# Kernel tuning notes

Hardware: AMD Instinct MI355X
Metric: run time of the kernel (lower is better)

Reference implementation:

```python
import jax, jax.numpy as jnp
import numpy as np

N_NODES = 100000


def gcn_conv(x, src, dst, deg_inv_sqrt, W, b, n):
    # GCNConv: h = D^{-1/2} (A + I) D^{-1/2} (x W) + b
    h = x @ W                                   # [N, out]
    norm = deg_inv_sqrt[src] * deg_inv_sqrt[dst]  # [E+N]
    msg = h[src] * norm[:, None]                # gather + scale
    out = jax.ops.segment_sum(msg, dst, num_segments=n)  # scatter-add
    return out + b


def setup_inputs() -> dict:
    key = jax.random.key(0)
    k1, k2, k3, k4 = jax.random.split(key, 4)
    N, E, IN, H, C = N_NODES, 1600000, 256, 128, 16
    x = jax.random.normal(k1, (N, IN), dtype=jnp.float32)
    edge_index = jax.random.randint(k2, (2, E), 0, N, dtype=jnp.int64)
    W1 = jax.random.normal(k3, (IN, H), dtype=jnp.float32) * (1.0 / np.sqrt(IN))
    b1 = jnp.zeros((H,), dtype=jnp.float32)
    W2 = jax.random.normal(k4, (H, C), dtype=jnp.float32) * (1.0 / np.sqrt(H))
    b2 = jnp.zeros((C,), dtype=jnp.float32)
    return {"x": x, "edge_index": edge_index, "W1": W1, "b1": b1, "W2": W2, "b2": b2}


def reference(x, edge_index, W1, b1, W2, b2):
    n = x.shape[0]
    loop = jnp.arange(n, dtype=edge_index.dtype)
    src = jnp.concatenate([edge_index[0], loop])  # add self-loops
    dst = jnp.concatenate([edge_index[1], loop])
    deg = jax.ops.segment_sum(jnp.ones_like(src, dtype=x.dtype), dst, num_segments=n)
    deg_inv_sqrt = jax.lax.rsqrt(deg)  # deg >= 1 due to self-loops

    h = gcn_conv(x, src, dst, deg_inv_sqrt, W1, b1, n)
    h = jax.nn.relu(h)
    # dropout is identity in eval mode
    out = gcn_conv(h, src, dst, deg_inv_sqrt, W2, b2, n)
    return jax.nn.log_softmax(out, axis=1)
```

## Files before the change

kernel.cpp:

```cpp
#include <hip/hip_runtime.h>
#include <math.h>

#define IN_DIM 256
#define H_DIM  128
#define C_DIM  16
#define BK_SHIFT 8
#define BK_CAP   6144
#define CHUNK    4096

typedef __attribute__((ext_vector_type(8))) short bf16x8;
typedef __attribute__((ext_vector_type(4))) float f32x4;

__device__ __forceinline__ ushort f2bf(float f) {
    uint u = __float_as_uint(f);
    u += 0x7fffu + ((u >> 16) & 1u);
    return (ushort)(u >> 16);
}
__device__ __forceinline__ float bflo(uint v) { return __uint_as_float(v << 16); }
__device__ __forceinline__ float bfhi(uint v) { return __uint_as_float(v & 0xffff0000u); }
__device__ __forceinline__ uint pk2(float a, float b) {
    return (uint)f2bf(a) | ((uint)f2bf(b) << 16);
}

__global__ void k_zero(int* __restrict__ p, int n) {
    int i = blockIdx.x * blockDim.x + threadIdx.x;
    if (i < n) p[i] = 0;
}

__global__ __launch_bounds__(256) void k_part(const int* __restrict__ esrc, const int* __restrict__ edst, int E,
                                              int* __restrict__ bcnt, int2* __restrict__ part) {
    __shared__ int sh_cnt[512];
    __shared__ int sh_base[512];
    __shared__ int sh_gbase[512];
    __shared__ int sh_scan[256];
    __shared__ int2 sh_rec[CHUNK];
    int t = threadIdx.x;
    int c0 = blockIdx.x * CHUNK;
    int cnt = min(CHUNK, E - c0);
    sh_cnt[t] = 0; sh_cnt[t + 256] = 0;
    __syncthreads();
    int srcv[16], dstv[16], lrank[16];
#pragma unroll
    for (int j = 0; j < 16; j++) {
        int li = j * 256 + t;
        if (li < cnt) {
            srcv[j] = esrc[c0 + li]; dstv[j] = edst[c0 + li];
            lrank[j] = atomicAdd(&sh_cnt[dstv[j] >> BK_SHIFT], 1);
        }
    }
    __syncthreads();
    int pairsum = sh_cnt[2 * t] + sh_cnt[2 * t + 1];
    sh_scan[t] = pairsum;
    __syncthreads();
    for (int off = 1; off < 256; off <<= 1) {
        int x = 0;
        if (t >= off) x = sh_scan[t - off];
        __syncthreads();
        if (t >= off) sh_scan[t] += x;
        __syncthreads();
    }
    int excl = sh_scan[t] - pairsum;
    sh_base[2 * t] = excl;
    sh_base[2 * t + 1] = excl + sh_cnt[2 * t];
    __syncthreads();
    for (int b = t; b < 512; b += 256) {
        int c = sh_cnt[b];
        if (c > 0) sh_gbase[b] = atomicAdd(&bcnt[b], c);
    }
#pragma unroll
    for (int j = 0; j < 16; j++) {
        int li = j * 256 + t;
        if (li < cnt) {
            int b = dstv[j] >> BK_SHIFT;
            sh_rec[sh_base[b] + lrank[j]] = make_int2(srcv[j], dstv[j]);
        }
    }
    __syncthreads();
    for (int idx = t; idx < cnt; idx += 256) {
        int2 r = sh_rec[idx];
        int b = r.y >> BK_SHIFT;
        int pos = sh_gbase[b] + (idx - sh_base[b]);
        if (pos < BK_CAP) part[(size_t)b * BK_CAP + pos] = r;
    }
}

__global__ __launch_bounds__(256) void k_bdeg(const int* __restrict__ bcnt, const int2* __restrict__ part,
                                              int* __restrict__ deg, float* __restrict__ dis, int N) {
    __shared__ int hist[256];
    int b = blockIdx.x, t = threadIdx.x;
    hist[t] = 0;
    __syncthreads();
    int cnt = bcnt[b];
    const int2* bp = &part[(size_t)b * BK_CAP];
    for (int idx = t; idx < cnt; idx += 256)
        atomicAdd(&hist[bp[idx].y & 255], 1);
    __syncthreads();
    int node = b * 256 + t;
    if (node < N) {
        deg[node] = hist[t];
        dis[node] = rsqrtf((float)(hist[t] + 1));
    }
}

__global__ void k_scanA(const int* __restrict__ deg, int* __restrict__ bsums, int N) {
    __shared__ int sh[256];
    int b = blockIdx.x, t = threadIdx.x;
    int i0 = b * 2048 + t * 8;
    int s = 0;
#pragma unroll
    for (int j = 0; j < 8; j++) { int i = i0 + j; s += (i < N) ? deg[i] : 0; }
    sh[t] = s; __syncthreads();
    for (int off = 128; off > 0; off >>= 1) {
        if (t < off) sh[t] += sh[t + off];
        __syncthreads();
    }
    if (t == 0) bsums[b] = sh[0];
}

__global__ void k_scanB(int* __restrict__ bsums, int nb, int* __restrict__ offsets, int N) {
    if (threadIdx.x == 0 && blockIdx.x == 0) {
        int run = 0;
        for (int b = 0; b < nb; b++) { int v = bsums[b]; bsums[b] = run; run += v; }
        offsets[N] = run;
    }
}

__global__ void k_scanC(const int* __restrict__ deg, const int* __restrict__ bsums,
                        int* __restrict__ offsets, int N) {
    __shared__ int sh[256];
    int b = blockIdx.x, t = threadIdx.x;
    int base = bsums[b];
    int i0 = b * 2048 + t * 8;
    int v[8], loc[8]; int s = 0;
#pragma unroll
    for (int j = 0; j < 8; j++) { int i = i0 + j; v[j] = (i < N) ? deg[i] : 0; loc[j] = s; s += v[j]; }
    sh[t] = s; __syncthreads();
    for (int off = 1; off < 256; off <<= 1) {
        int x = 0;
        if (t >= off) x = sh[t - off];
        __syncthreads();
        if (t >= off) sh[t] += x;
        __syncthreads();
    }
    int tb = base + ((t > 0) ? sh[t - 1] : 0);
#pragma unroll
    for (int j = 0; j < 8; j++) {
        int i = i0 + j;
        if (i < N) offsets[i] = tb + loc[j];
    }
}

__global__ __launch_bounds__(256) void k_bsort(const int* __restrict__ bcnt, const int2* __restrict__ part,
                                               const float* __restrict__ dis, const int* __restrict__ offsets,
                                               int2* __restrict__ csr) {
    __shared__ int hist[256];
    __shared__ int run[256];
    __shared__ int2 srt[BK_CAP];
    int b = blockIdx.x, t = threadIdx.x;
    hist[t] = 0;
    __syncthreads();
    int cnt = min(bcnt[b], BK_CAP);
    const int2* bp = &part[(size_t)b * BK_CAP];
    for (int idx = t; idx < cnt; idx += 256)
        atomicAdd(&hist[bp[idx].y & 255], 1);
    __syncthreads();
    int v = hist[t];
    run[t] = v;
    __syncthreads();
    for (int off = 1; off < 256; off <<= 1) {
        int x = 0;
        if (t >= off) x = run[t - off];
        __syncthreads();
        if (t >= off) run[t] += x;
        __syncthreads();
    }
    int start = run[t] - v;
    __syncthreads();
    run[t] = start;
    __syncthreads();
    for (int idx = t; idx < cnt; idx += 256) {
        int2 r = bp[idx];
        int n = r.y & 255;
        int lpos = atomicAdd(&run[n], 1);
        float w = dis[r.x];
        srt[lpos] = make_int2(r.x, __float_as_int(w));
    }
    __syncthreads();
    int segbase = offsets[b * 256];
    for (int idx = t; idx < cnt; idx += 256)
        csr[segbase + idx] = srt[idx];
}

__global__ void k_w1cast(const float* __restrict__ W1, ushort* __restrict__ W1T) {
    int n = blockIdx.x, k = threadIdx.x;
    W1T[n * 256 + k] = f2bf(W1[k * 128 + n]);
}

__global__ __launch_bounds__(256) void k_gemm1(const float* __restrict__ x,
                                               const ushort* __restrict__ W1T,
                                               ushort* __restrict__ h1, int N) {
    __shared__ ushort Al[128 * 64];
    __shared__ ushort Bl[128 * 64];
    int tid = threadIdx.x;
    int lane = tid & 63, wid = tid >> 6;
    int wr = wid >> 1, wc = wid & 1;
    int r0 = blockIdx.x * 128;
    int row16 = lane & 15, kgrp = lane >> 4;

    f32x4 acc[4][4];
#pragma unroll
    for (int i = 0; i < 4; i++)
#pragma unroll
        for (int j = 0; j < 4; j++) acc[i][j] = (f32x4){0.f, 0.f, 0.f, 0.f};

    int srow = tid >> 1, shalf = tid & 1;

    for (int k0 = 0; k0 < 256; k0 += 64) {
        {
            int gr = r0 + srow;
            float4 f[8];
            if (gr < N) {
                const float* xp = &x[(size_t)gr * 256 + k0 + shalf * 32];
#pragma unroll
                for (int j = 0; j < 8; j++) f[j] = *(const float4*)&xp[j * 4];
            } else {
#pragma unroll
                for (int j = 0; j < 8; j++) f[j] = make_float4(0.f, 0.f, 0.f, 0.f);
            }
#pragma unroll
            for (int j = 0; j < 4; j++) {
                uint4 w;
                w.x = pk2(f[2 * j].x, f[2 * j].y);
                w.y = pk2(f[2 * j].z, f[2 * j].w);
                w.z = pk2(f[2 * j + 1].x, f[2 * j + 1].y);
                w.w = pk2(f[2 * j + 1].z, f[2 * j + 1].w);
                int idx = (srow * 64 + shalf * 32 + j * 8) ^ ((srow & 7) << 3);
                *(uint4*)&Al[idx] = w;
            }
        }
        {
            const ushort* wp = &W1T[srow * 256 + k0 + shalf * 32];
#pragma unroll
            for (int j = 0; j < 4; j++) {
                uint4 w = *(const uint4*)&wp[j * 8];
                int idx = (srow * 64 + shalf * 32 + j * 8) ^ ((srow & 7) << 3);
                *(uint4*)&Bl[idx] = w;
            }
        }
        __syncthreads();
#pragma unroll
        for (int kk = 0; kk < 2; kk++) {
            bf16x8 a[4], b[4];
#pragma unroll
            for (int mi = 0; mi < 4; mi++) {
                int r = wr * 64 + mi * 16 + row16;
                a[mi] = *(const bf16x8*)&Al[(r * 64 + kk * 32 + kgrp * 8) ^ ((r & 7) << 3)];
            }
#pragma unroll
            for (int ni = 0; ni < 4; ni++) {
                int c = wc * 64 + ni * 16 + row16;
                b[ni] = *(const bf16x8*)&Bl[(c * 64 + kk * 32 + kgrp * 8) ^ ((c & 7) << 3)];
            }
#pragma unroll
            for (int mi = 0; mi < 4; mi++)
#pragma unroll
                for (int ni = 0; ni < 4; ni++)
                    acc[mi][ni] = __builtin_amdgcn_mfma_f32_16x16x32_bf16(
                        a[mi], b[ni], acc[mi][ni], 0, 0, 0);
        }
        __syncthreads();
    }
#pragma unroll
    for (int mi = 0; mi < 4; mi++) {
        int rbase = r0 + wr * 64 + mi * 16 + kgrp * 4;
#pragma unroll
        for (int ni = 0; ni < 4; ni++) {
            int col = wc * 64 + ni * 16 + row16;
#pragma unroll
            for (int r = 0; r < 4; r++) {
                int gr = rbase + r;
                if (gr < N) h1[(size_t)gr * 128 + col] = f2bf(acc[mi][ni][r]);
            }
        }
    }
}

__global__ __launch_bounds__(256) void k_agg1(const ushort* __restrict__ h1,
                                              const float* __restrict__ dis,
                                              const int* __restrict__ off,
                                              const int2* __restrict__ csr,
                                              const float* __restrict__ b1,
                                              const float* __restrict__ W2,
                                              ushort* __restrict__ h2, int N) {
    __shared__ float sh[4][128];
    int wave = threadIdx.x >> 6;
    int lane = threadIdx.x & 63;
    int node = blockIdx.x * 4 + wave;
    if (node >= N) return;

    int grp = lane >> 4, c = lane & 15;
    float w2r[32];
#pragma unroll
    for (int j = 0; j < 32; j++) w2r[j] = W2[(grp * 32 + j) * 16 + c];
    float2 bl = *(const float2*)&b1[lane * 2];

    float dd = dis[node];
    const uint* hp = (const uint*)h1;
    uint a = hp[(size_t)node * 64 + lane];
    float accx = bflo(a) * dd, accy = bfhi(a) * dd;

    int p0 = off[node], p1 = off[node + 1];
    for (int pb = p0; pb < p1; pb += 64) {
        int rem64 = p1 - pb;
        int cnt = rem64 < 64 ? rem64 : 64;
        int s = 0; float w = 0.f;
        if (lane < cnt) { int2 e = csr[pb + lane]; s = e.x; w = __int_as_float(e.y); }
        int j = 0;
        for (; j + 8 <= cnt; j += 8) {
            uint v[8]; float ww[8];
#pragma unroll
            for (int u = 0; u < 8; u++) {
                int ss = __shfl(s, j + u);
                ww[u] = __shfl(w, j + u);
                v[u] = hp[(size_t)ss * 64 + lane];
            }
#pragma unroll
            for (int u = 0; u < 8; u++) {
                accx += bflo(v[u]) * ww[u];
                accy += bfhi(v[u]) * ww[u];
            }
        }
        int rem = cnt - j;
        if (rem) {
            uint v[8]; float ww[8];
#pragma unroll
            for (int u = 0; u < 8; u++) {
                int ss = __shfl(s, j + u);
                float t = __shfl(w, j + u);
                ww[u] = (u < rem) ? t : 0.f;
                v[u] = (u < rem) ? hp[(size_t)ss * 64 + lane] : 0u;
            }
#pragma unroll
            for (int u = 0; u < 8; u++) {
                accx += bflo(v[u]) * ww[u];
                accy += bfhi(v[u]) * ww[u];
            }
        }
    }
    accx = fmaxf(accx * dd + bl.x, 0.f);
    accy = fmaxf(accy * dd + bl.y, 0.f);
    sh[wave][lane * 2]     = accx;
    sh[wave][lane * 2 + 1] = accy;
    float cs = 0.f;
#pragma unroll
    for (int j = 0; j < 32; j++) cs += sh[wave][grp * 32 + j] * w2r[j];
    cs += __shfl_xor(cs, 16);
    cs += __shfl_xor(cs, 32);
    if (lane < 16) h2[(size_t)node * 16 + lane] = f2bf(cs);
}

__global__ __launch_bounds__(256) void k_final(const ushort* __restrict__ h2,
                                               const float* __restrict__ b2,
                                               const float* __restrict__ dis,
                                               const int* __restrict__ off,
                                               const int2* __restrict__ csr,
                                               float* __restrict__ out, int N) {
    int g = threadIdx.x >> 2;
    int q = threadIdx.x & 3;
    int node = blockIdx.x * 64 + g;
    if (node >= N) return;
    float dd = dis[node];
    uint2 v0 = *(const uint2*)&h2[(size_t)node * 16 + q * 4];
    float a0 = bflo(v0.x) * dd, a1 = bfhi(v0.x) * dd;
    float a2 = bflo(v0.y) * dd, a3 = bfhi(v0.y) * dd;
    int p0 = off[node], p1 = off[node + 1];
    for (int pb = p0; pb < p1; pb += 4) {
        int rem4 = p1 - pb;
        int cnt = rem4 < 4 ? rem4 : 4;
        int s = 0; float w = 0.f;
        if (q < cnt) { int2 e = csr[pb + q]; s = e.x; w = __int_as_float(e.y); }
        uint2 vv[4]; float ww[4];
#pragma unroll
        for (int u = 0; u < 4; u++) {
            int ss = __shfl(s, u, 4);
            float t = __shfl(w, u, 4);
            ww[u] = (u < cnt) ? t : 0.f;
            if (u < cnt) vv[u] = *(const uint2*)&h2[(size_t)ss * 16 + q * 4];
            else         vv[u] = make_uint2(0u, 0u);
        }
#pragma unroll
        for (int u = 0; u < 4; u++) {
            a0 += bflo(vv[u].x) * ww[u]; a1 += bfhi(vv[u].x) * ww[u];
            a2 += bflo(vv[u].y) * ww[u]; a3 += bfhi(vv[u].y) * ww[u];
        }
    }
    a0 = a0 * dd + b2[q * 4 + 0];
    a1 = a1 * dd + b2[q * 4 + 1];
    a2 = a2 * dd + b2[q * 4 + 2];
    a3 = a3 * dd + b2[q * 4 + 3];
    float m = fmaxf(fmaxf(a0, a1), fmaxf(a2, a3));
    m = fmaxf(m, __shfl_xor(m, 1, 4));
    m = fmaxf(m, __shfl_xor(m, 2, 4));
    float s4 = expf(a0 - m) + expf(a1 - m) + expf(a2 - m) + expf(a3 - m);
    s4 += __shfl_xor(s4, 1, 4);
    s4 += __shfl_xor(s4, 2, 4);
    float l = m + logf(s4);
    f32x4 o = {a0 - l, a1 - l, a2 - l, a3 - l};
    *(f32x4*)&out[(size_t)node * 16 + q * 4] = o;
}

extern "C" void kernel_launch(void* const* d_in, const int* in_sizes, int n_in,
                              void* d_out, int out_size, void* d_ws, size_t ws_size,
                              hipStream_t stream) {
    const float* x    = (const float*)d_in[0];
    const int*   eidx = (const int*)d_in[1];
    const float* W1   = (const float*)d_in[2];
    const float* b1   = (const float*)d_in[3];
    const float* W2   = (const float*)d_in[4];
    const float* b2   = (const float*)d_in[5];
    float* out = (float*)d_out;

    int N = in_sizes[0] / IN_DIM;
    int E = in_sizes[1] / 2;
    const int* esrc = eidx;
    const int* edst = eidx + E;

    char* ws = (char*)d_ws;
    size_t wo = 0;
    auto alloc = [&](size_t bytes) -> void* {
        void* p = ws + wo;
        wo = (wo + bytes + 255) & ~(size_t)255;
        return p;
    };
    int NB = (N + 255) >> 8;

    int*    deg     = (int*)alloc((size_t)N * 4);
    float*  dis     = (float*)alloc((size_t)N * 4);
    int*    offsets = (int*)alloc((size_t)(N + 1) * 4);
    int*    bsums   = (int*)alloc(256 * 4);
    int*    bcnt    = (int*)alloc(512 * 4);
    int2*   part    = (int2*)alloc((size_t)NB * BK_CAP * 8);
    int2*   csr     = (int2*)alloc((size_t)E * 8);
    ushort* W1T     = (ushort*)alloc((size_t)IN_DIM * H_DIM * 2);
    ushort* h1      = (ushort*)alloc((size_t)N * H_DIM * 2);
    ushort* h2      = (ushort*)alloc((size_t)N * C_DIM * 2);

    int nb_scan = (N + 2047) / 2048;

    k_zero  <<<2, 256, 0, stream>>>(bcnt, 512);
    k_part  <<<(E + CHUNK - 1) / CHUNK, 256, 0, stream>>>(esrc, edst, E, bcnt, part);
    k_bdeg  <<<NB, 256, 0, stream>>>(bcnt, part, deg, dis, N);
    k_scanA <<<nb_scan, 256, 0, stream>>>(deg, bsums, N);
    k_scanB <<<1, 64, 0, stream>>>(bsums, nb_scan, offsets, N);
    k_scanC <<<nb_scan, 256, 0, stream>>>(deg, bsums, offsets, N);
    k_bsort <<<NB, 256, 0, stream>>>(bcnt, part, dis, offsets, csr);
    k_w1cast<<<H_DIM, IN_DIM, 0, stream>>>(W1, W1T);

    k_gemm1 <<<(N + 127) / 128, 256, 0, stream>>>(x, W1T, h1, N);
    k_agg1  <<<(N + 3) / 4, 256, 0, stream>>>(h1, dis, offsets, csr, b1, W2, h2, N);
    k_final <<<(N + 63) / 64, 256, 0, stream>>>(h2, b2, dis, offsets, csr, out, N);
}
```

Baseline: 191.0 us.

## Collapse degree and scan kernels into bucket scan, store CSR as src-only

Replaces the per-node degree kernel and the three-kernel prefix scan with a single-block scan over bucket counts. The bucket sort kernel now computes each node's degree, inverse sqrt degree and CSR offset from its local histogram. CSR entries shrink from (src, weight) pairs to src indices only, and the aggregation kernels gather dis[src] on the fly. This removes several launches and a full pass over the partitioned edges, and halves CSR traffic, at the cost of an extra random gather of dis per edge in both aggregation passes.

```diff
diff --git a/kernel.cpp b/kernel.cpp
--- a/kernel.cpp
+++ b/kernel.cpp
@@ -84,78 +84,34 @@
     }
 }
 
-__global__ __launch_bounds__(256) void k_bdeg(const int* __restrict__ bcnt, const int2* __restrict__ part,
-                                              int* __restrict__ deg, float* __restrict__ dis, int N) {
-    __shared__ int hist[256];
-    int b = blockIdx.x, t = threadIdx.x;
-    hist[t] = 0;
-    __syncthreads();
-    int cnt = bcnt[b];
-    const int2* bp = &part[(size_t)b * BK_CAP];
-    for (int idx = t; idx < cnt; idx += 256)
-        atomicAdd(&hist[bp[idx].y & 255], 1);
-    __syncthreads();
-    int node = b * 256 + t;
-    if (node < N) {
-        deg[node] = hist[t];
-        dis[node] = rsqrtf((float)(hist[t] + 1));
-    }
-}
-
-__global__ void k_scanA(const int* __restrict__ deg, int* __restrict__ bsums, int N) {
-    __shared__ int sh[256];
-    int b = blockIdx.x, t = threadIdx.x;
-    int i0 = b * 2048 + t * 8;
-    int s = 0;
-#pragma unroll
-    for (int j = 0; j < 8; j++) { int i = i0 + j; s += (i < N) ? deg[i] : 0; }
-    sh[t] = s; __syncthreads();
-    for (int off = 128; off > 0; off >>= 1) {
-        if (t < off) sh[t] += sh[t + off];
-        __syncthreads();
-    }
-    if (t == 0) bsums[b] = sh[0];
-}
-
-__global__ void k_scanB(int* __restrict__ bsums, int nb, int* __restrict__ offsets, int N) {
-    if (threadIdx.x == 0 && blockIdx.x == 0) {
-        int run = 0;
-        for (int b = 0; b < nb; b++) { int v = bsums[b]; bsums[b] = run; run += v; }
-        offsets[N] = run;
-    }
-}
-
-__global__ void k_scanC(const int* __restrict__ deg, const int* __restrict__ bsums,
-                        int* __restrict__ offsets, int N) {
-    __shared__ int sh[256];
-    int b = blockIdx.x, t = threadIdx.x;
-    int base = bsums[b];
-    int i0 = b * 2048 + t * 8;
-    int v[8], loc[8]; int s = 0;
-#pragma unroll
-    for (int j = 0; j < 8; j++) { int i = i0 + j; v[j] = (i < N) ? deg[i] : 0; loc[j] = s; s += v[j]; }
-    sh[t] = s; __syncthreads();
+__global__ __launch_bounds__(256) void k_bscan(const int* __restrict__ bcnt, int* __restrict__ bkbase,
+                                               int* __restrict__ offsets, int N) {
+    __shared__ int sh_scan[256];
+    int t = threadIdx.x;
+    int a0 = bcnt[2 * t], a1 = bcnt[2 * t + 1];
+    int pairsum = a0 + a1;
+    sh_scan[t] = pairsum;
+    __syncthreads();
     for (int off = 1; off < 256; off <<= 1) {
         int x = 0;
-        if (t >= off) x = sh[t - off];
-        __syncthreads();
-        if (t >= off) sh[t] += x;
-        __syncthreads();
-    }
-    int tb = base + ((t > 0) ? sh[t - 1] : 0);
-#pragma unroll
-    for (int j = 0; j < 8; j++) {
-        int i = i0 + j;
-        if (i < N) offsets[i] = tb + loc[j];
-    }
-}
-
-__global__ __launch_bounds__(256) void k_bsort(const int* __restrict__ bcnt, const int2* __restrict__ part,
-                                               const float* __restrict__ dis, const int* __restrict__ offsets,
-                                               int2* __restrict__ csr) {
+        if (t >= off) x = sh_scan[t - off];
+        __syncthreads();
+        if (t >= off) sh_scan[t] += x;
+        __syncthreads();
+    }
+    int excl = sh_scan[t] - pairsum;
+    bkbase[2 * t] = excl;
+    bkbase[2 * t + 1] = excl + a0;
+    if (t == 255) offsets[N] = sh_scan[255];
+}
+
+__global__ __launch_bounds__(256) void k_bsort(const int* __restrict__ bcnt, const int* __restrict__ bkbase,
+                                               const int2* __restrict__ part,
+                                               float* __restrict__ dis, int* __restrict__ offsets,
+                                               int* __restrict__ csr, int N) {
     __shared__ int hist[256];
     __shared__ int run[256];
-    __shared__ int2 srt[BK_CAP];
+    __shared__ int srt[BK_CAP];
     int b = blockIdx.x, t = threadIdx.x;
     hist[t] = 0;
     __syncthreads();
@@ -175,20 +131,23 @@
         __syncthreads();
     }
     int start = run[t] - v;
+    int base = bkbase[b];
+    int node = b * 256 + t;
+    if (node < N) {
+        dis[node] = rsqrtf((float)(v + 1));
+        offsets[node] = base + start;
+    }
     __syncthreads();
     run[t] = start;
     __syncthreads();
     for (int idx = t; idx < cnt; idx += 256) {
         int2 r = bp[idx];
-        int n = r.y & 255;
-        int lpos = atomicAdd(&run[n], 1);
-        float w = dis[r.x];
-        srt[lpos] = make_int2(r.x, __float_as_int(w));
-    }
-    __syncthreads();
-    int segbase = offsets[b * 256];
+        int lpos = atomicAdd(&run[r.y & 255], 1);
+        srt[lpos] = r.x;
+    }
+    __syncthreads();
     for (int idx = t; idx < cnt; idx += 256)
-        csr[segbase + idx] = srt[idx];
+        csr[base + idx] = srt[idx];
 }
 
 __global__ void k_w1cast(const float* __restrict__ W1, ushort* __restrict__ W1T) {
@@ -288,7 +247,7 @@
 __global__ __launch_bounds__(256) void k_agg1(const ushort* __restrict__ h1,
                                               const float* __restrict__ dis,
                                               const int* __restrict__ off,
-                                              const int2* __restrict__ csr,
+                                              const int* __restrict__ csr,
                                               const float* __restrict__ b1,
                                               const float* __restrict__ W2,
                                               ushort* __restrict__ h2, int N) {
@@ -314,7 +273,7 @@
         int rem64 = p1 - pb;
         int cnt = rem64 < 64 ? rem64 : 64;
         int s = 0; float w = 0.f;
-        if (lane < cnt) { int2 e = csr[pb + lane]; s = e.x; w = __int_as_float(e.y); }
+        if (lane < cnt) { s = csr[pb + lane]; w = dis[s]; }
         int j = 0;
         for (; j + 8 <= cnt; j += 8) {
             uint v[8]; float ww[8];
@@ -363,7 +322,7 @@
                                                const float* __restrict__ b2,
                                                const float* __restrict__ dis,
                                                const int* __restrict__ off,
-                                               const int2* __restrict__ csr,
+                                               const int* __restrict__ csr,
                                                float* __restrict__ out, int N) {
     int g = threadIdx.x >> 2;
     int q = threadIdx.x & 3;
@@ -378,7 +337,7 @@
         int rem4 = p1 - pb;
         int cnt = rem4 < 4 ? rem4 : 4;
         int s = 0; float w = 0.f;
-        if (q < cnt) { int2 e = csr[pb + q]; s = e.x; w = __int_as_float(e.y); }
+        if (q < cnt) { s = csr[pb + q]; w = dis[s]; }
         uint2 vv[4]; float ww[4];
 #pragma unroll
         for (int u = 0; u < 4; u++) {
@@ -434,26 +393,20 @@
     };
     int NB = (N + 255) >> 8;
 
-    int*    deg     = (int*)alloc((size_t)N * 4);
     float*  dis     = (float*)alloc((size_t)N * 4);
     int*    offsets = (int*)alloc((size_t)(N + 1) * 4);
-    int*    bsums   = (int*)alloc(256 * 4);
     int*    bcnt    = (int*)alloc(512 * 4);
+    int*    bkbase  = (int*)alloc(512 * 4);
     int2*   part    = (int2*)alloc((size_t)NB * BK_CAP * 8);
-    int2*   csr     = (int2*)alloc((size_t)E * 8);
+    int*    csr     = (int*)alloc((size_t)E * 4);
     ushort* W1T     = (ushort*)alloc((size_t)IN_DIM * H_DIM * 2);
     ushort* h1      = (ushort*)alloc((size_t)N * H_DIM * 2);
     ushort* h2      = (ushort*)alloc((size_t)N * C_DIM * 2);
 
-    int nb_scan = (N + 2047) / 2048;
-
     k_zero  <<<2, 256, 0, stream>>>(bcnt, 512);
     k_part  <<<(E + CHUNK - 1) / CHUNK, 256, 0, stream>>>(esrc, edst, E, bcnt, part);
-    k_bdeg  <<<NB, 256, 0, stream>>>(bcnt, part, deg, dis, N);
-    k_scanA <<<nb_scan, 256, 0, stream>>>(deg, bsums, N);
-    k_scanB <<<1, 64, 0, stream>>>(bsums, nb_scan, offsets, N);
-    k_scanC <<<nb_scan, 256, 0, stream>>>(deg, bsums, offsets, N);
-    k_bsort <<<NB, 256, 0, stream>>>(bcnt, part, dis, offsets, csr);
+    k_bscan <<<1, 256, 0, stream>>>(bcnt, bkbase, offsets, N);
+    k_bsort <<<NB, 256, 0, stream>>>(bcnt, bkbase, part, dis, offsets, csr, N);
     k_w1cast<<<H_DIM, IN_DIM, 0, stream>>>(W1, W1T);
 
     k_gemm1 <<<(N + 127) / 128, 256, 0, stream>>>(x, W1T, h1, N);
```

Measured after the change: 175.4 us. 1.09x faster.
